# Performance work log

Hardware: AMD Instinct MI355X
Metric: run time of the kernel (lower is better)

The kernel has to match this reference:

```python
import math
import jax, jax.numpy as jnp
import numpy as np

D_MODEL = 512
NHEAD = 8
FACTOR = 5


def setup_inputs() -> dict:
    key = jax.random.key(0)
    ks = jax.random.split(key, 16)
    B, L, D = 4, 2048, D_MODEL
    s = 0.02
    inp = {
        "queries": jax.random.normal(ks[0], (B, L, D), jnp.float32),
        "keys": jax.random.normal(ks[1], (B, L, D), jnp.float32),
        "values": jax.random.normal(ks[2], (B, L, D), jnp.float32),
        "Wq": jax.random.normal(ks[3], (D, D), jnp.float32) * s,
        "bq": jnp.zeros((D,), jnp.float32),
        "Wk": jax.random.normal(ks[4], (D, D), jnp.float32) * s,
        "bk": jnp.zeros((D,), jnp.float32),
        "Wv": jax.random.normal(ks[5], (D, D), jnp.float32) * s,
        "bv": jnp.zeros((D,), jnp.float32),
        "Wo": jax.random.normal(ks[6], (D, D), jnp.float32) * s,
        "bo": jnp.zeros((D,), jnp.float32),
    }
    # sample_k = factor * ceil(ln(L_K+1)) = 5*8 = 40, shared across batch & heads
    U = min(FACTOR * int(np.ceil(np.log(L + 1))), L)
    inp["index_sample"] = jax.random.randint(ks[7], (L, U), 0, L, jnp.int32)
    return inp


def reference(queries, keys, values, Wq, bq, Wk, bk, Wv, bv, Wo, bo, index_sample):
    B, LQ, D = queries.shape
    LK = keys.shape[1]
    H = NHEAD
    dk = D // H

    # projections (torch Linear: x @ W.T + b), split into heads -> (B,H,L,dk)
    def proj(x, W, b):
        y = x @ W.T + b
        return y.reshape(B, -1, H, dk).transpose(0, 2, 1, 3)

    Q = proj(queries, Wq, bq)
    K = proj(keys, Wk, bk)
    V = proj(values, Wv, bv)

    U = min(FACTOR * int(np.ceil(np.log(LK + 1))), LK)  # sampled keys per query
    u = min(FACTOR * int(np.ceil(np.log(LQ + 1))), LQ)  # top queries kept

    # initial context: mean of V broadcast over queries  (B,H,LQ,dk)
    context = jnp.broadcast_to(V.mean(axis=2, keepdims=True), (B, H, LQ, dk))

    if LQ > u:
        # gather sampled keys: (B,H,LQ,U,dk)  [dominant memory traffic]
        K_sample = K[:, :, index_sample, :]
        # per-query scores against sampled keys: (B,H,LQ,U)
        QK_sample = jnp.einsum('bhqd,bhqud->bhqu', Q, K_sample)
        # sparsity measure M = max - mean
        M = QK_sample.max(axis=-1) - QK_sample.sum(axis=-1) / LK  # (B,H,LQ)
        M_top = jax.lax.top_k(M, u)[1]  # (B,H,u)

        # gather selected queries: (B,H,u,dk)
        Q_reduce = jnp.take_along_axis(Q, M_top[..., None], axis=2)
        scores = jnp.einsum('bhud,bhkd->bhuk', Q_reduce, K) / math.sqrt(dk)
        attn = jax.nn.softmax(scores, axis=-1)  # dropout = eval mode (identity)
        context_in = jnp.einsum('bhuk,bhkd->bhud', attn, V)  # (B,H,u,dk)

        # scatter attended rows back into the mean context
        bi = jnp.arange(B)[:, None, None]
        hi = jnp.arange(H)[None, :, None]
        context = context.at[bi, hi, M_top].set(context_in)
    else:
        scores = jnp.einsum('bhqd,bhkd->bhqk', Q, K) / math.sqrt(dk)
        attn = jax.nn.softmax(scores, axis=-1)
        context = jnp.einsum('bhqk,bhkd->bhqd', attn, V)

    context = context.transpose(0, 2, 1, 3).reshape(B, LQ, D)
    return context @ Wo.T + bo
```

## Files before the change

kernel.cpp:

```cpp
#include <hip/hip_runtime.h>
#include <math.h>

constexpr int Bn  = 4;
constexpr int Ln  = 2048;
constexpr int Dn  = 512;
constexpr int Hn  = 8;
constexpr int DKn = 64;
constexpr int US  = 40;
constexpr int UT  = 40;
constexpr int NCk = 32;
constexpr int CKn = 64;

typedef unsigned short ushort_t;

__device__ __forceinline__ ushort_t f2bf_rne(float x) {
  unsigned u = __float_as_uint(x);
  unsigned r = u + 0x7fffu + ((u >> 16) & 1u);
  return (ushort_t)(r >> 16);
}
__device__ __forceinline__ float bf2f(ushort_t h) {
  return __uint_as_float(((unsigned)h) << 16);
}

__global__ __launch_bounds__(256) void split_in(const float* __restrict__ X,
                                                ushort_t* __restrict__ A)
{
  int i = blockIdx.x * 256 + threadIdx.x;
  int m = i >> 7, c4 = (i & 127) << 2;
  float4 x = *reinterpret_cast<const float4*>(&X[(size_t)m * 512 + c4]);
  ushort_t h0 = f2bf_rne(x.x), h1 = f2bf_rne(x.y), h2 = f2bf_rne(x.z), h3 = f2bf_rne(x.w);
  ushort_t l0 = f2bf_rne(x.x - bf2f(h0)), l1 = f2bf_rne(x.y - bf2f(h1));
  ushort_t l2 = f2bf_rne(x.z - bf2f(h2)), l3 = f2bf_rne(x.w - bf2f(h3));
  *reinterpret_cast<ushort4*>(&A[(size_t)m * 1024 + c4])       = make_ushort4(h0, h1, h2, h3);
  *reinterpret_cast<ushort4*>(&A[(size_t)m * 1024 + 512 + c4]) = make_ushort4(l0, l1, l2, l3);
}

__global__ __launch_bounds__(256) void split_w(const float* __restrict__ W,
                                               ushort_t* __restrict__ Wc)
{
  int i = blockIdx.x * 256 + threadIdx.x;
  int n = i >> 7, c4 = (i & 127) << 2;
  float4 x = *reinterpret_cast<const float4*>(&W[(size_t)n * 512 + c4]);
  ushort_t h0 = f2bf_rne(x.x), h1 = f2bf_rne(x.y), h2 = f2bf_rne(x.z), h3 = f2bf_rne(x.w);
  ushort_t l0 = f2bf_rne(x.x - bf2f(h0)), l1 = f2bf_rne(x.y - bf2f(h1));
  ushort_t l2 = f2bf_rne(x.z - bf2f(h2)), l3 = f2bf_rne(x.w - bf2f(h3));
  ushort4 hv = make_ushort4(h0, h1, h2, h3);
  ushort4 lv = make_ushort4(l0, l1, l2, l3);
  *reinterpret_cast<ushort4*>(&Wc[(size_t)n * 1536 + c4])        = hv;
  *reinterpret_cast<ushort4*>(&Wc[(size_t)n * 1536 + 512 + c4])  = lv;
  *reinterpret_cast<ushort4*>(&Wc[(size_t)n * 1536 + 1024 + c4]) = hv;
}

using bf16x8 = short __attribute__((ext_vector_type(8)));
using f32x4  = float __attribute__((ext_vector_type(4)));

__device__ __forceinline__ void gload_lds16(const void* g, void* l) {
  __builtin_amdgcn_global_load_lds((const __attribute__((address_space(1))) void*)g,
                                   (__attribute__((address_space(3))) void*)l, 16, 0, 0);
}

__global__ __launch_bounds__(256) void gemm3_bf16(const ushort_t* __restrict__ Ast,
    const ushort_t* __restrict__ Bst, const float* __restrict__ bias,
    float* __restrict__ out)
{
  __shared__ __attribute__((aligned(16))) ushort_t sA[64 * 64];
  __shared__ __attribute__((aligned(16))) ushort_t sB[128 * 64];
  const int tid = threadIdx.x;
  const int w = tid >> 6, lane = tid & 63;
  const int m0 = blockIdx.y * 64, n0 = blockIdx.x * 128;
  const int wr = w >> 1, wc = w & 1;
  const int r16 = lane & 15, ko = (lane >> 4) * 8;

  f32x4 acc[2][4];
#pragma unroll
  for (int m = 0; m < 2; ++m)
#pragma unroll
    for (int n = 0; n < 4; ++n) acc[m][n] = (f32x4){0.f, 0.f, 0.f, 0.f};

  for (int k0 = 0; k0 < 1536; k0 += 64) {
    const int ka0 = (k0 < 1024) ? (k0 & 511) : (k0 - 512);
    __syncthreads();
#pragma unroll
    for (int i = 0; i < 2; ++i) {
      int e = i * 256 + tid, r = e >> 3, c8 = e & 7;
      gload_lds16(Ast + (size_t)(m0 + r) * 1024 + ka0 + c8 * 8,
                  (void*)(sA + (size_t)(i * 256 + w * 64) * 8));
    }
#pragma unroll
    for (int i = 0; i < 4; ++i) {
      int e = i * 256 + tid, r = e >> 3, c8 = e & 7;
      gload_lds16(Bst + (size_t)(n0 + r) * 1536 + k0 + c8 * 8,
                  (void*)(sB + (size_t)(i * 256 + w * 64) * 8));
    }
    __syncthreads();
#pragma unroll
    for (int kk = 0; kk < 64; kk += 32) {
      bf16x8 a[2], b[4];
#pragma unroll
      for (int m = 0; m < 2; ++m)
        a[m] = *reinterpret_cast<const bf16x8*>(&sA[(wr * 32 + m * 16 + r16) * 64 + kk + ko]);
#pragma unroll
      for (int n = 0; n < 4; ++n)
        b[n] = *reinterpret_cast<const bf16x8*>(&sB[(wc * 64 + n * 16 + r16) * 64 + kk + ko]);
#pragma unroll
      for (int m = 0; m < 2; ++m)
#pragma unroll
        for (int n = 0; n < 4; ++n)
          acc[m][n] = __builtin_amdgcn_mfma_f32_16x16x32_bf16(a[m], b[n], acc[m][n], 0, 0, 0);
    }
  }

#pragma unroll
  for (int m = 0; m < 2; ++m) {
#pragma unroll
    for (int n = 0; n < 4; ++n) {
#pragma unroll
      for (int r = 0; r < 4; ++r) {
        int row = m0 + wr * 32 + m * 16 + (lane >> 4) * 4 + r;
        int col = n0 + wc * 64 + n * 16 + (lane & 15);
        float v = acc[m][n][r] + bias[col];
        int b = row >> 11, l = row & 2047, h = col >> 6, dd = col & 63;
        out[(size_t)((b * Hn + h) * Ln + l) * DKn + dd] = v;
      }
    }
  }
}

__global__ __launch_bounds__(256) void vmean1(const float* __restrict__ Vf,
                                              float* __restrict__ part)
{
  int bh = blockIdx.x, ch = blockIdx.y;
  int t = threadIdx.x;
  int d4 = t & 15, ls = t >> 4;
  const float* base = Vf + ((size_t)bh * Ln + ch * 128) * DKn;
  float4 s = make_float4(0.f, 0.f, 0.f, 0.f);
#pragma unroll
  for (int i = 0; i < 8; ++i) {
    float4 x = *reinterpret_cast<const float4*>(&base[(size_t)(ls + i * 16) * DKn + d4 * 4]);
    s.x += x.x; s.y += x.y; s.z += x.z; s.w += x.w;
  }
  __shared__ float4 red[16][16];
  red[ls][d4] = s;
  __syncthreads();
  if (t < 64) {
    int dd = t & 15, g = t >> 4;
    float4 a = red[g * 4 + 0][dd], b = red[g * 4 + 1][dd];
    float4 c = red[g * 4 + 2][dd], d = red[g * 4 + 3][dd];
    red[g * 4][dd] = make_float4(a.x + b.x + c.x + d.x, a.y + b.y + c.y + d.y,
                                 a.z + b.z + c.z + d.z, a.w + b.w + c.w + d.w);
  }
  __syncthreads();
  if (t < 16) {
    float4 a = red[0][t], b = red[4][t], c = red[8][t], d = red[12][t];
    float4 r = make_float4(a.x + b.x + c.x + d.x, a.y + b.y + c.y + d.y,
                           a.z + b.z + c.z + d.z, a.w + b.w + c.w + d.w);
    *reinterpret_cast<float4*>(&part[((size_t)(bh * 16 + ch)) * DKn + t * 4]) = r;
  }
}

__global__ __launch_bounds__(64) void vmean2(const float* __restrict__ part,
                                             float* __restrict__ meanV)
{
  int bh = blockIdx.x, d = threadIdx.x;
  float s = 0.f;
#pragma unroll
  for (int ch = 0; ch < 16; ++ch) s += part[((size_t)(bh * 16 + ch)) * DKn + d];
  meanV[bh * DKn + d] = s * (1.f / 2048.f);
}

__global__ __launch_bounds__(256) void qk_sample_m2(const float* __restrict__ Qf,
    const float* __restrict__ Kf, const int* __restrict__ isamp,
    float* __restrict__ Mout)
{
  int wq = blockIdx.x * 4 + (threadIdx.x >> 6);
  int lane = threadIdx.x & 63;
  int g = lane >> 4, s = lane & 15;
  int bh = wq >> 11, q = wq & 2047;
  const float* Kb = Kf + (size_t)bh * Ln * DKn;
  float4 qv = *reinterpret_cast<const float4*>(&Qf[(size_t)(bh * Ln + q) * DKn + s * 4]);
  float mx = -INFINITY, sm = 0.f;
#pragma unroll
  for (int p = 0; p < 10; ++p) {
    int u = p * 4 + g;
    int idx = isamp[q * US + u];
    float4 kv = *reinterpret_cast<const float4*>(&Kb[(size_t)idx * DKn + s * 4]);
    float d = qv.x * kv.x + qv.y * kv.y + qv.z * kv.z + qv.w * kv.w;
#pragma unroll
    for (int off = 1; off < 16; off <<= 1) d += __shfl_xor(d, off);
    mx = fmaxf(mx, d);
    sm += d;
  }
#pragma unroll
  for (int off = 16; off <= 32; off <<= 1) {
    mx = fmaxf(mx, __shfl_xor(mx, off));
    sm += __shfl_xor(sm, off);
  }
  if (lane == 0) Mout[wq] = mx - sm * (1.f / 2048.f);
}

__global__ __launch_bounds__(256) void topk40(const float* __restrict__ Mv,
                                              int* __restrict__ Mtop)
{
  int bh = blockIdx.x, tid = threadIdx.x;
  __shared__ unsigned hist[256];
  __shared__ unsigned sfx[256];
  __shared__ unsigned prefix_s, k_s;
  __shared__ int outcnt, tiecnt;
  __shared__ int tlist[256];

  unsigned key[8];
#pragma unroll
  for (int i = 0; i < 8; ++i) {
    unsigned u = __float_as_uint(Mv[bh * Ln + tid + i * 256]);
    key[i] = (u & 0x80000000u) ? ~u : (u | 0x80000000u);
  }
  if (tid == 0) { prefix_s = 0u; k_s = UT; outcnt = 0; tiecnt = 0; }
  __syncthreads();

  for (int d = 24; d >= 0; d -= 8) {
    hist[tid] = 0u;
    __syncthreads();
    unsigned pref = prefix_s;
    unsigned mask = (d == 24) ? 0u : (0xFFFFFFFFu << (d + 8));
#pragma unroll
    for (int i = 0; i < 8; ++i)
      if ((key[i] & mask) == pref) atomicAdd(&hist[(key[i] >> d) & 255u], 1u);
    __syncthreads();
    sfx[tid] = hist[tid];
    __syncthreads();
    for (int off = 1; off < 256; off <<= 1) {
      unsigned add = (tid + off < 256) ? sfx[tid + off] : 0u;
      __syncthreads();
      sfx[tid] += add;
      __syncthreads();
    }
    unsigned k = k_s;
    unsigned nxt = (tid < 255) ? sfx[tid + 1] : 0u;
    if (sfx[tid] >= k && nxt < k) {
      prefix_s = pref | ((unsigned)tid << d);
      k_s = k - nxt;
    }
    __syncthreads();
  }

  unsigned T = prefix_s;
  int kf = (int)k_s;
#pragma unroll
  for (int i = 0; i < 8; ++i) {
    int idx = tid + i * 256;
    if (key[i] > T) {
      int s = atomicAdd(&outcnt, 1);
      Mtop[bh * UT + s] = idx;
    } else if (key[i] == T) {
      int s = atomicAdd(&tiecnt, 1);
      if (s < 256) tlist[s] = idx;
    }
  }
  __syncthreads();
  if (tid == 0) {
    int n = tiecnt < 256 ? tiecnt : 256;
    int basep = outcnt;
    for (int a = 0; a < kf; ++a) {
      int best = 1 << 30, bj = 0;
      for (int j = 0; j < n; ++j)
        if (tlist[j] < best) { best = tlist[j]; bj = j; }
      Mtop[bh * UT + basep + a] = best;
      tlist[bj] = 1 << 30;
    }
  }
}

__global__ __launch_bounds__(256) void attn_partial(const float* __restrict__ Qf,
    const float* __restrict__ Kf, const float* __restrict__ Vf,
    const int* __restrict__ Mtop, float* __restrict__ pmv,
    float* __restrict__ plv, float* __restrict__ pacc)
{
  const int bh = blockIdx.x, c = blockIdx.y;
  const int tid = threadIdx.x;
  const int w = tid >> 6, lane = tid & 63;
  __shared__ float sQ[UT][DKn];
  __shared__ float sS[UT][CKn];
  __shared__ float sK[CKn * DKn];

  for (int i = tid; i < UT * DKn; i += 256) {
    int r = i >> 6, d = i & 63;
    sQ[r][d] = Qf[(size_t)(bh * Ln + Mtop[bh * UT + r]) * DKn + d];
  }
  const float* Kc = Kf + (size_t)(bh * Ln + c * CKn) * DKn;
  for (int i = tid; i < CKn * DKn; i += 256) {
    int r = i >> 6, d = i & 63;
    sK[r * 64 + (d ^ ((r & 15) << 2))] = Kc[(size_t)r * DKn + d];
  }
  __syncthreads();

  for (int it = 0; it < 10; ++it) {
    int i = w + it * 4, kk = lane;
    float s = 0.f;
#pragma unroll
    for (int g = 0; g < 16; ++g) {
      float4 qv = *reinterpret_cast<const float4*>(&sQ[i][g * 4]);
      float4 kv = *reinterpret_cast<const float4*>(&sK[kk * 64 + ((g * 4) ^ ((kk & 15) << 2))]);
      s += qv.x * kv.x + qv.y * kv.y + qv.z * kv.z + qv.w * kv.w;
    }
    sS[i][kk] = s * 0.125f;
  }
  __syncthreads();

  for (int it = 0; it < 10; ++it) {
    int i = w + it * 4;
    float s0 = sS[i][lane];
    float mx = s0;
#pragma unroll
    for (int off = 32; off; off >>= 1) mx = fmaxf(mx, __shfl_xor(mx, off));
    float p0 = expf(s0 - mx);
    sS[i][lane] = p0;
    float ls = p0;
#pragma unroll
    for (int off = 32; off; off >>= 1) ls += __shfl_xor(ls, off);
    if (lane == 0) {
      pmv[(bh * NCk + c) * UT + i] = mx;
      plv[(bh * NCk + c) * UT + i] = ls;
    }
  }
  __syncthreads();

  const int ksub = lane >> 4, dq = lane & 15;
  const float* Vc = Vf + (size_t)(bh * Ln + c * CKn) * DKn;
  float4 acc[10];
#pragma unroll
  for (int t = 0; t < 10; ++t) acc[t] = make_float4(0.f, 0.f, 0.f, 0.f);
  for (int ko = 0; ko < 16; ++ko) {
    int kk = ko * 4 + ksub;
    float4 v4 = *reinterpret_cast<const float4*>(&Vc[(size_t)kk * DKn + dq * 4]);
#pragma unroll
    for (int t = 0; t < 10; ++t) {
      float wgt = sS[w + t * 4][kk];
      acc[t].x += wgt * v4.x; acc[t].y += wgt * v4.y;
      acc[t].z += wgt * v4.z; acc[t].w += wgt * v4.w;
    }
  }
#pragma unroll
  for (int t = 0; t < 10; ++t) {
#pragma unroll
    for (int off = 16; off <= 32; off <<= 1) {
      acc[t].x += __shfl_xor(acc[t].x, off);
      acc[t].y += __shfl_xor(acc[t].y, off);
      acc[t].z += __shfl_xor(acc[t].z, off);
      acc[t].w += __shfl_xor(acc[t].w, off);
    }
  }
  if (ksub == 0) {
#pragma unroll
    for (int t = 0; t < 10; ++t) {
      int i = w + t * 4;
      *reinterpret_cast<float4*>(&pacc[(size_t)((bh * NCk + c) * UT + i) * DKn + dq * 4]) = acc[t];
    }
  }
}

__global__ __launch_bounds__(256) void base_proj(const float* __restrict__ meanV,
    const float* __restrict__ Wo, const float* __restrict__ bo,
    float* __restrict__ base)
{
  int b = blockIdx.x, tid = threadIdx.x;
#pragma unroll
  for (int rep = 0; rep < 2; ++rep) {
    int n = tid + rep * 256;
    float s = bo[n];
#pragma unroll 8
    for (int g = 0; g < 128; ++g) {
      float4 wv = *reinterpret_cast<const float4*>(&Wo[(size_t)n * Dn + g * 4]);
      float4 mv = *reinterpret_cast<const float4*>(&meanV[b * Dn + g * 4]);
      s += wv.x * mv.x + wv.y * mv.y + wv.z * mv.z + wv.w * mv.w;
    }
    base[b * Dn + n] = s;
  }
}

__global__ __launch_bounds__(256) void base_fill(const float* __restrict__ base,
                                                 float* __restrict__ out)
{
  int idx = blockIdx.x * 256 + threadIdx.x;
  int row = idx >> 7, col4 = idx & 127;
  int b = row >> 11;
  reinterpret_cast<float4*>(out)[idx] =
      reinterpret_cast<const float4*>(base)[b * 128 + col4];
}

__global__ __launch_bounds__(256) void combine_scatter(const float* __restrict__ pmv,
    const float* __restrict__ plv, const float* __restrict__ pacc,
    const int* __restrict__ Mtop, const float* __restrict__ meanV,
    const float* __restrict__ Wo, float* __restrict__ out)
{
  int bi = blockIdx.x;
  int bh = bi / UT, i = bi % UT;
  int b = bh >> 3, h = bh & 7;
  int tid = threadIdx.x;
  __shared__ float v[DKn];
  if (tid < 64) {
    int d = tid;
    float mg = -INFINITY;
    for (int cc = 0; cc < NCk; ++cc) mg = fmaxf(mg, pmv[(bh * NCk + cc) * UT + i]);
    float den = 0.f, num = 0.f;
    for (int cc = 0; cc < NCk; ++cc) {
      float e = expf(pmv[(bh * NCk + cc) * UT + i] - mg);
      den += plv[(bh * NCk + cc) * UT + i] * e;
      num += e * pacc[(size_t)((bh * NCk + cc) * UT + i) * DKn + d];
    }
    v[d] = num / den - meanV[bh * DKn + d];
  }
  __syncthreads();
  int q = Mtop[bh * UT + i];
  float* orow = out + (size_t)(b * Ln + q) * Dn;
  const float* Wh = Wo + h * DKn;
#pragma unroll
  for (int rep = 0; rep < 2; ++rep) {
    int n = tid + rep * 256;
    float s = 0.f;
#pragma unroll
    for (int g = 0; g < 16; ++g) {
      float4 wv = *reinterpret_cast<const float4*>(&Wh[(size_t)n * Dn + g * 4]);
      float4 vv = *reinterpret_cast<const float4*>(&v[g * 4]);
      s += wv.x * vv.x + wv.y * vv.y + wv.z * vv.z + wv.w * vv.w;
    }
    atomicAdd(&orow[n], s);
  }
}

extern "C" void kernel_launch(void* const* d_in, const int* in_sizes, int n_in,
                              void* d_out, int out_size, void* d_ws, size_t ws_size,
                              hipStream_t stream)
{
  const float* queries = (const float*)d_in[0];
  const float* keys    = (const float*)d_in[1];
  const float* values  = (const float*)d_in[2];
  const float* Wq = (const float*)d_in[3];
  const float* bq = (const float*)d_in[4];
  const float* Wk = (const float*)d_in[5];
  const float* bk = (const float*)d_in[6];
  const float* Wv = (const float*)d_in[7];
  const float* bv = (const float*)d_in[8];
  const float* Wo = (const float*)d_in[9];
  const float* bo = (const float*)d_in[10];
  const int* isamp = (const int*)d_in[11];
  float* out = (float*)d_out;

  float* ws = (float*)d_ws;
  const size_t NBL = (size_t)Bn * Hn * Ln * DKn;
  float* Qf    = ws;
  float* Kf    = Qf + NBL;
  float* Vf    = Kf + NBL;
  float* meanV = Vf + NBL;
  float* Mv    = meanV + Bn * Hn * DKn;
  float* pmv   = Mv + Bn * Hn * Ln;
  float* plv   = pmv + Bn * Hn * NCk * UT;
  float* base  = plv + Bn * Hn * NCk * UT;
  int* Mtop    = (int*)(base + Bn * Dn);
  ushort_t* Acat = (ushort_t*)(Mtop + Bn * Hn * UT);
  ushort_t* Wcat = Acat + (size_t)8192 * 1024;
  float* vpart = (float*)(Wcat + (size_t)512 * 1536);
  float* pacc  = (float*)Acat;

  dim3 gg(4, 128);
  split_in<<<4096, 256, 0, stream>>>(queries, Acat);
  split_w<<<256, 256, 0, stream>>>(Wq, Wcat);
  gemm3_bf16<<<gg, 256, 0, stream>>>(Acat, Wcat, bq, Qf);
  split_in<<<4096, 256, 0, stream>>>(keys, Acat);
  split_w<<<256, 256, 0, stream>>>(Wk, Wcat);
  gemm3_bf16<<<gg, 256, 0, stream>>>(Acat, Wcat, bk, Kf);
  split_in<<<4096, 256, 0, stream>>>(values, Acat);
  split_w<<<256, 256, 0, stream>>>(Wv, Wcat);
  gemm3_bf16<<<gg, 256, 0, stream>>>(Acat, Wcat, bv, Vf);

  vmean1<<<dim3(Bn * Hn, 16), 256, 0, stream>>>(Vf, vpart);
  vmean2<<<Bn * Hn, 64, 0, stream>>>(vpart, meanV);
  qk_sample_m2<<<Bn * Hn * Ln / 4, 256, 0, stream>>>(Qf, Kf, isamp, Mv);
  topk40<<<Bn * Hn, 256, 0, stream>>>(Mv, Mtop);
  attn_partial<<<dim3(Bn * Hn, NCk), 256, 0, stream>>>(Qf, Kf, Vf, Mtop, pmv, plv, pacc);
  base_proj<<<Bn, 256, 0, stream>>>(meanV, Wo, bo, base);
  base_fill<<<4096, 256, 0, stream>>>(base, out);
  combine_scatter<<<Bn * Hn * UT, 256, 0, stream>>>(pmv, plv, pacc, Mtop, meanV, Wo, out);
}
```

Before: 377.1 us.

## Split combine/scatter into per-head combine and Wo-reusing scatter projection kernels

```diff
diff --git a/kernel.cpp b/kernel.cpp
--- a/kernel.cpp
+++ b/kernel.cpp
@@ -387,43 +387,70 @@
       reinterpret_cast<const float4*>(base)[b * 128 + col4];
 }
 
-__global__ __launch_bounds__(256) void combine_scatter(const float* __restrict__ pmv,
+__global__ __launch_bounds__(256) void combine_ctx(const float* __restrict__ pmv,
     const float* __restrict__ plv, const float* __restrict__ pacc,
-    const int* __restrict__ Mtop, const float* __restrict__ meanV,
-    const float* __restrict__ Wo, float* __restrict__ out)
-{
-  int bi = blockIdx.x;
-  int bh = bi / UT, i = bi % UT;
+    const float* __restrict__ meanV, float* __restrict__ ctxd)
+{
+  int bh = blockIdx.x, tid = threadIdx.x;
+  __shared__ float ew[UT][NCk];
+  __shared__ float den_s[UT];
+  if (tid < UT) {
+    float mg = -INFINITY;
+#pragma unroll
+    for (int cc = 0; cc < NCk; ++cc)
+      mg = fmaxf(mg, pmv[(bh * NCk + cc) * UT + tid]);
+    float den = 0.f;
+#pragma unroll
+    for (int cc = 0; cc < NCk; ++cc) {
+      float e = expf(pmv[(bh * NCk + cc) * UT + tid] - mg);
+      ew[tid][cc] = e;
+      den += plv[(bh * NCk + cc) * UT + tid] * e;
+    }
+    den_s[tid] = den;
+  }
+  __syncthreads();
+  for (int v = tid; v < UT * DKn; v += 256) {
+    int i = v >> 6, d = v & 63;
+    float num = 0.f;
+#pragma unroll
+    for (int cc = 0; cc < NCk; ++cc)
+      num += ew[i][cc] * pacc[(size_t)((bh * NCk + cc) * UT + i) * DKn + d];
+    ctxd[(size_t)(bh * UT + i) * DKn + d] = num / den_s[i] - meanV[bh * DKn + d];
+  }
+}
+
+__global__ __launch_bounds__(256) void scatter_proj(const float* __restrict__ ctxd,
+    const int* __restrict__ Mtop, const float* __restrict__ Wo,
+    float* __restrict__ out)
+{
+  int nc = blockIdx.x, bh = blockIdx.y;
   int b = bh >> 3, h = bh & 7;
   int tid = threadIdx.x;
-  __shared__ float v[DKn];
-  if (tid < 64) {
-    int d = tid;
-    float mg = -INFINITY;
-    for (int cc = 0; cc < NCk; ++cc) mg = fmaxf(mg, pmv[(bh * NCk + cc) * UT + i]);
-    float den = 0.f, num = 0.f;
-    for (int cc = 0; cc < NCk; ++cc) {
-      float e = expf(pmv[(bh * NCk + cc) * UT + i] - mg);
-      den += plv[(bh * NCk + cc) * UT + i] * e;
-      num += e * pacc[(size_t)((bh * NCk + cc) * UT + i) * DKn + d];
-    }
-    v[d] = num / den - meanV[bh * DKn + d];
-  }
-  __syncthreads();
-  int q = Mtop[bh * UT + i];
-  float* orow = out + (size_t)(b * Ln + q) * Dn;
-  const float* Wh = Wo + h * DKn;
-#pragma unroll
-  for (int rep = 0; rep < 2; ++rep) {
-    int n = tid + rep * 256;
+  __shared__ float sd[UT][DKn];
+  __shared__ int qidx[UT];
+  for (int v = tid; v < UT * DKn; v += 256)
+    sd[v >> 6][v & 63] = ctxd[(size_t)(bh * UT) * DKn + v];
+  if (tid < UT) qidx[tid] = Mtop[bh * UT + tid];
+  __syncthreads();
+
+  int n = nc * 64 + (tid & 63);
+  int i0 = tid >> 6;
+  const float* Wrow = Wo + (size_t)n * Dn + h * DKn;
+  float4 wv[16];
+#pragma unroll
+  for (int g = 0; g < 16; ++g)
+    wv[g] = *reinterpret_cast<const float4*>(&Wrow[g * 4]);
+
+#pragma unroll
+  for (int t = 0; t < 10; ++t) {
+    int i = i0 + t * 4;
     float s = 0.f;
 #pragma unroll
     for (int g = 0; g < 16; ++g) {
-      float4 wv = *reinterpret_cast<const float4*>(&Wh[(size_t)n * Dn + g * 4]);
-      float4 vv = *reinterpret_cast<const float4*>(&v[g * 4]);
-      s += wv.x * vv.x + wv.y * vv.y + wv.z * vv.z + wv.w * vv.w;
-    }
-    atomicAdd(&orow[n], s);
+      float4 dv = *reinterpret_cast<const float4*>(&sd[i][g * 4]);
+      s += wv[g].x * dv.x + wv[g].y * dv.y + wv[g].z * dv.z + wv[g].w * dv.w;
+    }
+    atomicAdd(&out[(size_t)(b * Ln + qidx[i]) * Dn + n], s);
   }
 }
 
@@ -456,7 +483,8 @@
   float* plv   = pmv + Bn * Hn * NCk * UT;
   float* base  = plv + Bn * Hn * NCk * UT;
   int* Mtop    = (int*)(base + Bn * Dn);
-  ushort_t* Acat = (ushort_t*)(Mtop + Bn * Hn * UT);
+  float* ctxd  = (float*)(Mtop + Bn * Hn * UT);
+  ushort_t* Acat = (ushort_t*)(ctxd + (size_t)Bn * Hn * UT * DKn);
   ushort_t* Wcat = Acat + (size_t)8192 * 1024;
   float* vpart = (float*)(Wcat + (size_t)512 * 1536);
   float* pacc  = (float*)Acat;
@@ -479,5 +507,6 @@
   attn_partial<<<dim3(Bn * Hn, NCk), 256, 0, stream>>>(Qf, Kf, Vf, Mtop, pmv, plv, pacc);
   base_proj<<<Bn, 256, 0, stream>>>(meanV, Wo, bo, base);
   base_fill<<<4096, 256, 0, stream>>>(base, out);
-  combine_scatter<<<Bn * Hn * UT, 256, 0, stream>>>(pmv, plv, pacc, Mtop, meanV, Wo, out);
-}
+  combine_ctx<<<Bn * Hn, 256, 0, stream>>>(pmv, plv, pacc, meanV, ctxd);
+  scatter_proj<<<dim3(8, Bn * Hn), 256, 0, stream>>>(ctxd, Mtop, Wo, out);
+}
```

New measurement: 355.2 us. 1.06x faster.
